# Kernel tuning notes

Measured on AMD Instinct MI355X. Metric: run time of the kernel, lower is better.

Reference implementation:

```python
import jax, jax.numpy as jnp
import numpy as np
import math

B, S, HID, H = 2, 2048, 2048, 16
D = HID // H  # head_dim = 128


def rotate_half(x):
    x1, x2 = x[..., : x.shape[-1] // 2], x[..., x.shape[-1] // 2:]
    return jnp.concatenate((-x2, x1), axis=-1)


def setup_inputs() -> dict:
    key = jax.random.key(0)
    ks = jax.random.split(key, 6)
    x = jax.random.normal(ks[0], (B, S, HID), dtype=jnp.float32)
    # learned projection weights (torch Linear: y = x @ W.T); store as [in, out]
    scale = 1.0 / math.sqrt(HID)
    Wq = jax.random.normal(ks[1], (HID, HID), dtype=jnp.float32) * scale
    Wk = jax.random.normal(ks[2], (HID, HID), dtype=jnp.float32) * scale
    Wv = jax.random.normal(ks[3], (HID, HID), dtype=jnp.float32) * scale
    Wo = jax.random.normal(ks[4], (HID, HID), dtype=jnp.float32) * scale
    # causal additive mask [1,1,S,S]
    causal = jnp.tril(jnp.ones((S, S), dtype=bool))
    attention_mask = jnp.where(causal, 0.0, -1e9).astype(jnp.float32)[None, None]
    # ALiBi bias: slope per head times key position, broadcast over queries
    slopes = 2.0 ** (-8.0 * (jnp.arange(1, H + 1, dtype=jnp.float32) / H))
    alibi = (-slopes[:, None] * jnp.arange(S, dtype=jnp.float32)[None, :])[None, :, None, :]  # [1,H,1,S]
    # RoPE tables broadcastable to [B,H,S,D]
    inv_freq = 1.0 / (10000.0 ** (jnp.arange(0, D // 2, dtype=jnp.float32) / (D // 2)))
    t = jnp.arange(S, dtype=jnp.float32)
    freqs = t[:, None] * inv_freq[None, :]            # [S, D/2]
    emb = jnp.concatenate((freqs, freqs), axis=-1)    # [S, D]
    freqs_cos = jnp.cos(emb)[None, None]              # [1,1,S,D]
    freqs_sin = jnp.sin(emb)[None, None]
    return {"x": x, "Wq": Wq, "Wk": Wk, "Wv": Wv, "Wo": Wo,
            "attention_mask": attention_mask, "alibi": alibi,
            "freqs_cos": freqs_cos, "freqs_sin": freqs_sin}


def reference(x, Wq, Wk, Wv, Wo, attention_mask, alibi, freqs_cos, freqs_sin):
    b, s, _ = x.shape
    def split_heads(y):
        return y.reshape(b, s, H, D).transpose(0, 2, 1, 3)  # [B,H,S,D]
    q = split_heads(x @ Wq)
    k = split_heads(x @ Wk)
    v = split_heads(x @ Wv)
    q = q * freqs_cos + rotate_half(q) * freqs_sin
    k = k * freqs_cos + rotate_half(k) * freqs_sin
    scores = jnp.einsum('bhqd,bhkd->bhqk', q, k) / math.sqrt(D)
    scores = scores + attention_mask + alibi
    attn = jax.nn.softmax(scores, axis=-1)  # dropout p=0 (eval) -> identity
    out = jnp.einsum('bhqk,bhkd->bhqd', attn, v)
    out = out.transpose(0, 2, 1, 3).reshape(b, s, HID)
    return out @ Wo
```

## Files before the change

### kernel.cpp

```cpp
#include <hip/hip_runtime.h>

#define S_LEN   2048
#define HEADS   16
#define HID_DIM 2048
#define HEAD_D  128
#define BATCH   2

typedef __bf16          bf16x8 __attribute__((ext_vector_type(8)));
typedef unsigned short  u16x8  __attribute__((ext_vector_type(8)));
typedef unsigned short  u16x4  __attribute__((ext_vector_type(4)));
typedef float           f32x4  __attribute__((ext_vector_type(4)));

__device__ __forceinline__ unsigned short f2bf(float f) {
  unsigned u = __builtin_bit_cast(unsigned, f);
  u += 0x7FFFu + ((u >> 16) & 1u);
  return (unsigned short)(u >> 16);
}
__device__ __forceinline__ float bf2f(unsigned short s) {
  unsigned u = ((unsigned)s) << 16;
  return __builtin_bit_cast(float, u);
}

__device__ __forceinline__ f32x4 mfma16(u16x8 a, u16x8 b, f32x4 c) {
  return __builtin_amdgcn_mfma_f32_16x16x32_bf16(
      __builtin_bit_cast(bf16x8, a), __builtin_bit_cast(bf16x8, b), c, 0, 0, 0);
}

__device__ __forceinline__ void async_load16(const void* g, void* l) {
  __builtin_amdgcn_global_load_lds(
      (const __attribute__((address_space(1))) void*)g,
      (__attribute__((address_space(3))) void*)l, 16, 0, 0);
}

__global__ __launch_bounds__(256) void cvt_bf16(const float* __restrict__ in,
                                                unsigned short* __restrict__ out,
                                                int n8) {
  for (int i = blockIdx.x * blockDim.x + threadIdx.x; i < n8;
       i += gridDim.x * blockDim.x) {
    const float4* p = (const float4*)in + 2L * i;
    float4 a = p[0], b = p[1];
    u16x8 v;
    v[0] = f2bf(a.x); v[1] = f2bf(a.y); v[2] = f2bf(a.z); v[3] = f2bf(a.w);
    v[4] = f2bf(b.x); v[5] = f2bf(b.y); v[6] = f2bf(b.z); v[7] = f2bf(b.w);
    ((u16x8*)out)[i] = v;
  }
}

__global__ __launch_bounds__(256) void transpose_cvt(const float* __restrict__ W,
                                                     unsigned short* __restrict__ Wt,
                                                     int dim) {
  __shared__ float tile[32][33];
  const int bx = blockIdx.x * 32, by = blockIdx.y * 32;
  const int tx = threadIdx.x, ty = threadIdx.y;
#pragma unroll
  for (int i = 0; i < 32; i += 8)
    tile[ty + i][tx] = W[(long)(by + ty + i) * dim + bx + tx];
  __syncthreads();
#pragma unroll
  for (int i = 0; i < 32; i += 8)
    Wt[(long)(bx + ty + i) * dim + by + tx] = f2bf(tile[tx][ty + i]);
}

__global__ __launch_bounds__(256) void transpose_v(const unsigned short* __restrict__ V,
                                                   unsigned short* __restrict__ Vt) {
  __shared__ unsigned short tile[32][34];
  const int s0 = blockIdx.x * 32, d0 = blockIdx.y * 32, bh = blockIdx.z;
  const int b = bh >> 4, h = bh & 15;
  const int tx = threadIdx.x, ty = threadIdx.y;
#pragma unroll
  for (int i = 0; i < 32; i += 8)
    tile[ty + i][tx] =
        V[(long)(b * S_LEN + s0 + ty + i) * HID_DIM + h * HEAD_D + d0 + tx];
  __syncthreads();
#pragma unroll
  for (int i = 0; i < 32; i += 8)
    Vt[((long)bh * HEAD_D + d0 + ty + i) * S_LEN + s0 + tx] = tile[tx][ty + i];
}

__global__ __launch_bounds__(256) void rope_qk(unsigned short* __restrict__ Qb,
                                               unsigned short* __restrict__ Kb,
                                               const float* __restrict__ fcos,
                                               const float* __restrict__ fsin) {
  const long i = (long)blockIdx.x * blockDim.x + threadIdx.x;
  const int d = (int)(i & 63);
  const int h = (int)((i >> 6) & (HEADS - 1));
  const long row = i >> 10;
  const int s = (int)(row & (S_LEN - 1));
  const long base = row * HID_DIM + h * HEAD_D + d;
  const float c0 = fcos[s * HEAD_D + d], c1 = fcos[s * HEAD_D + d + 64];
  const float s0 = fsin[s * HEAD_D + d], s1 = fsin[s * HEAD_D + d + 64];
  const float q0 = bf2f(Qb[base]), q1 = bf2f(Qb[base + 64]);
  Qb[base]      = f2bf(q0 * c0 - q1 * s0);
  Qb[base + 64] = f2bf(q1 * c1 + q0 * s1);
  const float k0 = bf2f(Kb[base]), k1 = bf2f(Kb[base + 64]);
  Kb[base]      = f2bf(k0 * c0 - k1 * s0);
  Kb[base + 64] = f2bf(k1 * c1 + k0 * s1);
}

__global__ __launch_bounds__(256) void gemm_bt2(
    const unsigned short* __restrict__ A,
    const unsigned short* __restrict__ Bt0,
    unsigned short* __restrict__ Cb0,
    float* __restrict__ Cf,
    int M, int N, int K, int nbx, long zsB, long zsC) {
  __shared__ __align__(16) unsigned short Alds[2][128 * 32];
  __shared__ __align__(16) unsigned short Blds[2][128 * 32];
  const int t = threadIdx.x;
  const int lane = t & 63;
  const int w = t >> 6;
  const int wr = w >> 1, wc = w & 1;
  const int l15 = lane & 15, l4 = lane >> 4;

  const int nwg = gridDim.x;
  const int bid = blockIdx.x;
  const int sw = (bid & 7) * (nwg >> 3) + (bid >> 3);
  const int nby = M >> 7;
  const int z = sw / (nbx * nby);
  const int rem = sw - z * nbx * nby;
  const int by = rem / nbx;
  const int bx = rem - by * nbx;

  const unsigned short* Bt = Bt0 + (long)z * zsB;
  unsigned short* Cb = Cb0 ? Cb0 + (long)z * zsC : nullptr;

  f32x4 acc[4][4] = {};

  const long rowA = (long)by * 128 + (t >> 2);
  const long rowB = (long)bx * 128 + (t >> 2);
  const int kcol = (t & 3) * 8;
  const unsigned short* aSrc = A + rowA * K + kcol;
  const unsigned short* bSrc = Bt + rowB * K + kcol;
  const long skip = 64L * K;

  const int aBase = (wr * 64 + l15) * 32 + l4 * 8;
  const int bBase = (wc * 64 + l15) * 32 + l4 * 8;

#define STAGE(buf, kt) do {                                              \
    async_load16(aSrc + (kt),        (char*)(&Alds[buf][0]) + t * 16);   \
    async_load16(aSrc + (kt) + skip, (char*)(&Alds[buf][0]) + 4096 + t * 16); \
    async_load16(bSrc + (kt),        (char*)(&Blds[buf][0]) + t * 16);   \
    async_load16(bSrc + (kt) + skip, (char*)(&Blds[buf][0]) + 4096 + t * 16); \
  } while (0)

  STAGE(0, 0);
  asm volatile("s_waitcnt vmcnt(0)" ::: "memory");
  __builtin_amdgcn_s_barrier();

  int cur = 0;
  for (int kt = 0; kt < K; kt += 32) {
    if (kt + 32 < K) STAGE(cur ^ 1, kt + 32);
    const unsigned short* Ab = &Alds[cur][0];
    const unsigned short* Bb = &Blds[cur][0];
    u16x8 af[4], bfv[4];
#pragma unroll
    for (int m = 0; m < 4; ++m) af[m] = *(const u16x8*)&Ab[aBase + m * 512];
#pragma unroll
    for (int n = 0; n < 4; ++n) bfv[n] = *(const u16x8*)&Bb[bBase + n * 512];
#pragma unroll
    for (int m = 0; m < 4; ++m)
#pragma unroll
      for (int n = 0; n < 4; ++n)
        acc[m][n] = mfma16(af[m], bfv[n], acc[m][n]);
    __builtin_amdgcn_sched_barrier(0);
    __syncthreads();
    cur ^= 1;
  }
#undef STAGE

  const long orow = (long)by * 128 + wr * 64 + l4 * 4;
  const long ocol = (long)bx * 128 + wc * 64 + l15;
#pragma unroll
  for (int m = 0; m < 4; ++m)
#pragma unroll
    for (int n = 0; n < 4; ++n)
#pragma unroll
      for (int r = 0; r < 4; ++r) {
        const long row = orow + m * 16 + r;
        const long col = ocol + n * 16;
        if (Cb) Cb[row * N + col] = f2bf(acc[m][n][r]);
        else    Cf[row * N + col] = acc[m][n][r];
      }
}

__global__ __launch_bounds__(256) void attn_fwd4(const unsigned short* __restrict__ Q,
                                                 const unsigned short* __restrict__ K,
                                                 const unsigned short* __restrict__ Vt,
                                                 const float* __restrict__ alibi,
                                                 unsigned short* __restrict__ O) {
  __shared__ __align__(16) unsigned short Kl[2][32 * 128];
  __shared__ __align__(16) unsigned short Vl[2][64 * 64];
  __shared__ __align__(16) unsigned short Pl[4][32][40];
  const int t = threadIdx.x;
  const int lane = t & 63;
  const int w = t >> 6;
  const int l15 = lane & 15, l4 = lane >> 4;

  const int bid = blockIdx.x;
  const int half = bid >> 8, r0 = bid & 255;
  const int bh = r0 & 31;
  const int qt = half ? (15 - (r0 >> 5)) : (r0 >> 5);
  const int b = bh >> 4, h = bh & 15;
  const int q0b = qt * 128;
  const int q0 = q0b + w * 32;
  const float nslope = alibi[h * S_LEN + 1];
  const float scale = 0.08838834764831845f;

  const long rowbase = ((long)b * S_LEN) * HID_DIM + h * HEAD_D;
  const long vtbase  = ((long)bh * HEAD_D) * S_LEN;

  u16x8 qf[2][4];
  {
    const unsigned short* qp = Q + rowbase + (long)(q0 + l15) * HID_DIM + l4 * 8;
#pragma unroll
    for (int m = 0; m < 2; ++m)
#pragma unroll
      for (int ds = 0; ds < 4; ++ds)
        qf[m][ds] = *(const u16x8*)(qp + (long)m * 16 * HID_DIM + ds * 32);
  }

  f32x4 acc[2][8] = {};
  float m_r[2] = {-1e30f, -1e30f};
  float l_r[2] = {0.f, 0.f};

  int dd, rw, cbl;
  dd = 16 * t;        rw = dd >> 8; cbl = (dd & 255) ^ ((rw & 7) << 4);
  const unsigned short* ksrc0 = K + rowbase + (long)rw * HID_DIM + (cbl >> 1);
  dd = 4096 + 16 * t; rw = dd >> 8; cbl = (dd & 255) ^ ((rw & 7) << 4);
  const unsigned short* ksrc1 = K + rowbase + (long)rw * HID_DIM + (cbl >> 1);
  dd = 16 * t;        rw = dd >> 7; cbl = (dd & 127) ^ ((rw & 3) << 4);
  const unsigned short* vsrc0 =
      Vt + vtbase + (long)(2 * rw + (cbl >> 6)) * S_LEN + ((cbl & 63) >> 1);
  dd = 4096 + 16 * t; rw = dd >> 7; cbl = (dd & 127) ^ ((rw & 3) << 4);
  const unsigned short* vsrc1 =
      Vt + vtbase + (long)(2 * rw + (cbl >> 6)) * S_LEN + ((cbl & 63) >> 1);

#define ASTAGE(buf, kt_) do {                                             \
    const long kadd = (long)(kt_) * 32 * HID_DIM;                         \
    async_load16(ksrc0 + kadd, (char*)(&Kl[buf][0]) + 16 * t);            \
    async_load16(ksrc1 + kadd, (char*)(&Kl[buf][0]) + 4096 + 16 * t);     \
    async_load16(vsrc0 + (kt_) * 32, (char*)(&Vl[buf][0]) + 16 * t);      \
    async_load16(vsrc1 + (kt_) * 32, (char*)(&Vl[buf][0]) + 4096 + 16 * t); \
  } while (0)

  const int ntB = qt * 4 + 4;
  const int mykt = q0 >> 5;

  ASTAGE(0, 0);
  __syncthreads();

  int cur = 0;
  for (int kt = 0; kt < ntB; ++kt) {
    const int kb = kt * 32;
    if (kt + 1 < ntB) ASTAGE(cur ^ 1, kt + 1);
    if (kt <= mykt) {
      const char* Kc = (const char*)&Kl[cur][0];
      const char* Vc = (const char*)&Vl[cur][0];
      f32x4 sacc[2][2] = {};
#pragma unroll
      for (int ds = 0; ds < 4; ++ds) {
        u16x8 kfr[2];
#pragma unroll
        for (int n = 0; n < 2; ++n) {
          const int R = 16 * n + l15;
          const int cb = (ds * 64 + l4 * 16) ^ ((l15 & 7) << 4);
          kfr[n] = *(const u16x8*)(Kc + R * 256 + cb);
        }
#pragma unroll
        for (int n = 0; n < 2; ++n)
#pragma unroll
          for (int m = 0; m < 2; ++m)
            sacc[n][m] = mfma16(kfr[n], qf[m][ds], sacc[n][m]);
      }
#pragma unroll
      for (int m = 0; m < 2; ++m) {
        const int q = q0 + 16 * m + l15;
        float pv[2][4];
        float rmax = -1e30f;
#pragma unroll
        for (int n = 0; n < 2; ++n)
#pragma unroll
          for (int r = 0; r < 4; ++r) {
            const int k = kb + 16 * n + l4 * 4 + r;
            float v = sacc[n][m][r] * scale + nslope * (float)k;
            if (k > q) v = -1e30f;
            pv[n][r] = v;
            rmax = fmaxf(rmax, v);
          }
        rmax = fmaxf(rmax, __shfl_xor(rmax, 16, 64));
        rmax = fmaxf(rmax, __shfl_xor(rmax, 32, 64));
        const float mnew = fmaxf(m_r[m], rmax);
        const float sf = __expf(m_r[m] - mnew);
        m_r[m] = mnew;
        float rsum = 0.f;
#pragma unroll
        for (int n = 0; n < 2; ++n)
#pragma unroll
          for (int r = 0; r < 4; ++r) {
            pv[n][r] = __expf(pv[n][r] - mnew);
            rsum += pv[n][r];
          }
        rsum += __shfl_xor(rsum, 16, 64);
        rsum += __shfl_xor(rsum, 32, 64);
        l_r[m] = l_r[m] * sf + rsum;
        float sfo[4];
#pragma unroll
        for (int r = 0; r < 4; ++r) sfo[r] = __shfl(sf, l4 * 4 + r, 64);
#pragma unroll
        for (int dt = 0; dt < 8; ++dt)
#pragma unroll
          for (int r = 0; r < 4; ++r) acc[m][dt][r] *= sfo[r];
#pragma unroll
        for (int n = 0; n < 2; ++n) {
          u16x4 pk;
#pragma unroll
          for (int r = 0; r < 4; ++r) pk[r] = f2bf(pv[n][r]);
          *(u16x4*)&Pl[w][16 * m + l15][16 * n + l4 * 4] = pk;
        }
      }
      u16x8 pf[2];
#pragma unroll
      for (int m = 0; m < 2; ++m)
        pf[m] = *(const u16x8*)&Pl[w][16 * m + l15][l4 * 8];
#pragma unroll
      for (int dt = 0; dt < 8; ++dt) {
        const int d = dt * 16 + l15;
        const int vrow = d >> 1;
        const int cbv = (((d & 1) << 6) | (l4 << 4)) ^ ((vrow & 3) << 4);
        u16x8 vb = *(const u16x8*)(Vc + vrow * 128 + cbv);
#pragma unroll
        for (int m = 0; m < 2; ++m)
          acc[m][dt] = mfma16(pf[m], vb, acc[m][dt]);
      }
    }
    __builtin_amdgcn_sched_barrier(0);
    __syncthreads();
    cur ^= 1;
  }
#undef ASTAGE

#pragma unroll
  for (int m = 0; m < 2; ++m) {
    float linv[4];
#pragma unroll
    for (int r = 0; r < 4; ++r)
      linv[r] = 1.0f / __shfl(l_r[m], l4 * 4 + r, 64);
#pragma unroll
    for (int dt = 0; dt < 8; ++dt)
#pragma unroll
      for (int r = 0; r < 4; ++r) {
        const long row = q0 + 16 * m + l4 * 4 + r;
        O[rowbase + row * HID_DIM + dt * 16 + l15] = f2bf(acc[m][dt][r] * linv[r]);
      }
  }
}

extern "C" void kernel_launch(void* const* d_in, const int* in_sizes, int n_in,
                              void* d_out, int out_size, void* d_ws, size_t ws_size,
                              hipStream_t stream) {
  const float* x    = (const float*)d_in[0];
  const float* Wq   = (const float*)d_in[1];
  const float* Wk   = (const float*)d_in[2];
  const float* Wv   = (const float*)d_in[3];
  const float* Wo   = (const float*)d_in[4];
  const float* alibi = (const float*)d_in[6];
  const float* fcos  = (const float*)d_in[7];
  const float* fsin  = (const float*)d_in[8];

  char* ws = (char*)d_ws;
  unsigned short* xb  = (unsigned short*)(ws);
  unsigned short* wtq = (unsigned short*)(ws + (16L << 20));
  unsigned short* wtk = (unsigned short*)(ws + (24L << 20));
  unsigned short* wtv = (unsigned short*)(ws + (32L << 20));
  unsigned short* VtG = (unsigned short*)(ws + (24L << 20));
  unsigned short* Qb  = (unsigned short*)(ws + (40L << 20));
  unsigned short* Kb  = (unsigned short*)(ws + (56L << 20));
  unsigned short* Vb  = (unsigned short*)(ws + (72L << 20));

  const int M = BATCH * S_LEN;
  const int N = HID_DIM;
  const int K = HID_DIM;

  cvt_bf16<<<2048, 256, 0, stream>>>(x, xb, M * K / 8);

  dim3 tb(32, 8), tg(N / 32, K / 32);
  transpose_cvt<<<tg, tb, 0, stream>>>(Wq, wtq, N);
  transpose_cvt<<<tg, tb, 0, stream>>>(Wk, wtk, N);
  transpose_cvt<<<tg, tb, 0, stream>>>(Wv, wtv, N);

  gemm_bt2<<<3 * (M / 128) * (N / 128), 256, 0, stream>>>(
      xb, wtq, Qb, nullptr, M, N, K, N / 128,
      (long)HID_DIM * HID_DIM, (long)(8 << 20));

  rope_qk<<<(BATCH * S_LEN * HEADS * 64) / 256, 256, 0, stream>>>(Qb, Kb, fcos, fsin);

  transpose_v<<<dim3(S_LEN / 32, HEAD_D / 32, BATCH * HEADS), tb, 0, stream>>>(Vb, VtG);

  transpose_cvt<<<tg, tb, 0, stream>>>(Wo, wtq, N);

  attn_fwd4<<<512, 256, 0, stream>>>(Qb, Kb, VtG, alibi, xb);

  gemm_bt2<<<(M / 128) * (N / 128), 256, 0, stream>>>(
      xb, wtq, nullptr, (float*)d_out, M, N, K, N / 128, 0L, 0L);
}
```

Before: 324.4 us.

## Triple-buffer GEMM with LDS swizzle, XCD-aware attention mapping, fuse weight transposes

The GEMM moves from a double-buffered LDS pipeline to a three-stage one with two tiles in flight. It waits with a partial vmcnt and uses a single barrier per iteration. An XOR swizzle is applied to the LDS column layout to reduce bank conflicts on fragment reads. The attention kernel remaps block IDs so that each XCD handles a fixed set of batch-heads, which should improve L2 locality for K/V. The three QKV weight transposes are merged into one launch. The extra LDS buffer raises shared memory use per block, which could lower occupancy.

```diff
diff --git a/kernel.cpp b/kernel.cpp
--- a/kernel.cpp
+++ b/kernel.cpp
@@ -44,6 +44,26 @@
     v[4] = f2bf(b.x); v[5] = f2bf(b.y); v[6] = f2bf(b.z); v[7] = f2bf(b.w);
     ((u16x8*)out)[i] = v;
   }
+}
+
+__global__ __launch_bounds__(256) void transpose_cvt3(
+    const float* __restrict__ W0, const float* __restrict__ W1,
+    const float* __restrict__ W2, unsigned short* __restrict__ O0,
+    unsigned short* __restrict__ O1, unsigned short* __restrict__ O2,
+    int dim) {
+  __shared__ float tile[32][33];
+  const int z = blockIdx.z;
+  const float* W = (z == 0) ? W0 : (z == 1) ? W1 : W2;
+  unsigned short* Wt = (z == 0) ? O0 : (z == 1) ? O1 : O2;
+  const int bx = blockIdx.x * 32, by = blockIdx.y * 32;
+  const int tx = threadIdx.x, ty = threadIdx.y;
+#pragma unroll
+  for (int i = 0; i < 32; i += 8)
+    tile[ty + i][tx] = W[(long)(by + ty + i) * dim + bx + tx];
+  __syncthreads();
+#pragma unroll
+  for (int i = 0; i < 32; i += 8)
+    Wt[(long)(bx + ty + i) * dim + by + tx] = f2bf(tile[tx][ty + i]);
 }
 
 __global__ __launch_bounds__(256) void transpose_cvt(const float* __restrict__ W,
@@ -97,14 +117,14 @@
   Kb[base + 64] = f2bf(k1 * c1 + k0 * s1);
 }
 
-__global__ __launch_bounds__(256) void gemm_bt2(
+__global__ __launch_bounds__(256) void gemm_bt3(
     const unsigned short* __restrict__ A,
     const unsigned short* __restrict__ Bt0,
     unsigned short* __restrict__ Cb0,
     float* __restrict__ Cf,
     int M, int N, int K, int nbx, long zsB, long zsC) {
-  __shared__ __align__(16) unsigned short Alds[2][128 * 32];
-  __shared__ __align__(16) unsigned short Blds[2][128 * 32];
+  __shared__ __align__(16) unsigned short Alds[3][128 * 32];
+  __shared__ __align__(16) unsigned short Blds[3][128 * 32];
   const int t = threadIdx.x;
   const int lane = t & 63;
   const int w = t >> 6;
@@ -127,13 +147,14 @@
 
   const long rowA = (long)by * 128 + (t >> 2);
   const long rowB = (long)bx * 128 + (t >> 2);
-  const int kcol = (t & 3) * 8;
+  const int kcol = 8 * ((t & 3) ^ ((t >> 3) & 3));
   const unsigned short* aSrc = A + rowA * K + kcol;
   const unsigned short* bSrc = Bt + rowB * K + kcol;
   const long skip = 64L * K;
 
-  const int aBase = (wr * 64 + l15) * 32 + l4 * 8;
-  const int bBase = (wc * 64 + l15) * 32 + l4 * 8;
+  const int swz = (l4 ^ ((l15 >> 1) & 3)) * 8;
+  const int aBase = (wr * 64 + l15) * 32 + swz;
+  const int bBase = (wc * 64 + l15) * 32 + swz;
 
 #define STAGE(buf, kt) do {                                              \
     async_load16(aSrc + (kt),        (char*)(&Alds[buf][0]) + t * 16);   \
@@ -142,13 +163,19 @@
     async_load16(bSrc + (kt) + skip, (char*)(&Blds[buf][0]) + 4096 + t * 16); \
   } while (0)
 
+  const int KT = K >> 5;
   STAGE(0, 0);
-  asm volatile("s_waitcnt vmcnt(0)" ::: "memory");
-  __builtin_amdgcn_s_barrier();
+  STAGE(1, 32);
 
   int cur = 0;
-  for (int kt = 0; kt < K; kt += 32) {
-    if (kt + 32 < K) STAGE(cur ^ 1, kt + 32);
+  for (int it = 0; it < KT; ++it) {
+    if (it + 1 < KT) asm volatile("s_waitcnt vmcnt(4)" ::: "memory");
+    else             asm volatile("s_waitcnt vmcnt(0)" ::: "memory");
+    asm volatile("s_barrier" ::: "memory");
+    if (it + 2 < KT) {
+      const int nb = (cur + 2 >= 3) ? cur - 1 : cur + 2;
+      STAGE(nb, (it + 2) * 32);
+    }
     const unsigned short* Ab = &Alds[cur][0];
     const unsigned short* Bb = &Blds[cur][0];
     u16x8 af[4], bfv[4];
@@ -161,9 +188,7 @@
 #pragma unroll
       for (int n = 0; n < 4; ++n)
         acc[m][n] = mfma16(af[m], bfv[n], acc[m][n]);
-    __builtin_amdgcn_sched_barrier(0);
-    __syncthreads();
-    cur ^= 1;
+    cur = (cur + 1 >= 3) ? 0 : cur + 1;
   }
 #undef STAGE
 
@@ -182,7 +207,7 @@
       }
 }
 
-__global__ __launch_bounds__(256) void attn_fwd4(const unsigned short* __restrict__ Q,
+__global__ __launch_bounds__(256) void attn_fwd5(const unsigned short* __restrict__ Q,
                                                  const unsigned short* __restrict__ K,
                                                  const unsigned short* __restrict__ Vt,
                                                  const float* __restrict__ alibi,
@@ -196,9 +221,12 @@
   const int l15 = lane & 15, l4 = lane >> 4;
 
   const int bid = blockIdx.x;
-  const int half = bid >> 8, r0 = bid & 255;
-  const int bh = r0 & 31;
-  const int qt = half ? (15 - (r0 >> 5)) : (r0 >> 5);
+  const int xcd = bid & 7;
+  const int idx = bid >> 3;
+  const int qh = idx >> 4;
+  const int ql = idx & 15;
+  const int qt = (qh < 2) ? ql : (15 - ql);
+  const int bh = xcd * 4 + qh;
   const int b = bh >> 4, h = bh & 15;
   const int q0b = qt * 128;
   const int q0 = q0b + w * 32;
@@ -382,12 +410,11 @@
 
   cvt_bf16<<<2048, 256, 0, stream>>>(x, xb, M * K / 8);
 
-  dim3 tb(32, 8), tg(N / 32, K / 32);
-  transpose_cvt<<<tg, tb, 0, stream>>>(Wq, wtq, N);
-  transpose_cvt<<<tg, tb, 0, stream>>>(Wk, wtk, N);
-  transpose_cvt<<<tg, tb, 0, stream>>>(Wv, wtv, N);
-
-  gemm_bt2<<<3 * (M / 128) * (N / 128), 256, 0, stream>>>(
+  dim3 tb(32, 8);
+  transpose_cvt3<<<dim3(N / 32, K / 32, 3), tb, 0, stream>>>(
+      Wq, Wk, Wv, wtq, wtk, wtv, N);
+
+  gemm_bt3<<<3 * (M / 128) * (N / 128), 256, 0, stream>>>(
       xb, wtq, Qb, nullptr, M, N, K, N / 128,
       (long)HID_DIM * HID_DIM, (long)(8 << 20));
 
@@ -395,10 +422,10 @@
 
   transpose_v<<<dim3(S_LEN / 32, HEAD_D / 32, BATCH * HEADS), tb, 0, stream>>>(Vb, VtG);
 
-  transpose_cvt<<<tg, tb, 0, stream>>>(Wo, wtq, N);
-
-  attn_fwd4<<<512, 256, 0, stream>>>(Qb, Kb, VtG, alibi, xb);
-
-  gemm_bt2<<<(M / 128) * (N / 128), 256, 0, stream>>>(
+  transpose_cvt<<<dim3(N / 32, K / 32), tb, 0, stream>>>(Wo, wtq, N);
+
+  attn_fwd5<<<512, 256, 0, stream>>>(Qb, Kb, VtG, alibi, xb);
+
+  gemm_bt3<<<(M / 128) * (N / 128), 256, 0, stream>>>(
       xb, wtq, nullptr, (float*)d_out, M, N, K, N / 128, 0L, 0L);
 }
```

After: 318.8 us. No clear change (-1.7%).
